# Performance work log

Hardware: AMD Instinct MI355X
Metric: run time of the kernel (lower is better)

The kernel has to match this reference:

```python
import jax, jax.numpy as jnp
import numpy as np

LOG_2PI = float(np.log(2.0 * np.pi))


def setup_inputs() -> dict:
    key = jax.random.key(0)
    k1, k2, k3 = jax.random.split(key, 3)
    N, M, D = 8192, 4096, 784
    samples = jax.random.normal(k1, (N, D), dtype=jnp.float32)
    x = jax.random.normal(k2, (M, D), dtype=jnp.float32)
    # per-feature std, kept away from zero for numerical sanity
    std = jax.random.uniform(k3, (D,), dtype=jnp.float32, minval=0.5, maxval=1.5)
    return {"samples": samples, "x": x, "std": std}


def reference(samples, x, std):
    # Diagonal-Gaussian mixture log-prob:
    #   logp[n, m] = sum_d [ -0.5*((s_nd - x_md)/std_d)^2 - 0.5*log(2*pi) - log(std_d) ]
    # computed via the ||u||^2 + ||v||^2 - 2 u.v identity on std-scaled vectors
    # (mathematically identical to the torch broadcast, without the (N,M,D) tensor).
    N, D = samples.shape
    M = x.shape[0]
    u = samples / std  # (N, D)
    v = x / std        # (M, D)
    sq_dist = (
        jnp.sum(u * u, axis=1)[:, None]
        + jnp.sum(v * v, axis=1)[None, :]
        - 2.0 * jnp.einsum("nd,md->nm", u, v)
    )  # (N, M)
    log_const = -0.5 * D * LOG_2PI - jnp.sum(jnp.log(std))
    log_prob = -0.5 * sq_dist + log_const  # (N, M)
    # logsumexp over mixture components, minus log(M)
    return jax.nn.logsumexp(log_prob, axis=1) - jnp.log(jnp.asarray(M, dtype=samples.dtype))
```

## Files before the change

### kernel.cpp

```cpp
#include <hip/hip_runtime.h>
#include <cstdint>
#include <cstddef>


#define N_ROWS 8192
#define M_ROWS 4096
#define D_DIM  784
#define KPB    896
#define LOG2PI 1.8378770664093453f
#define LOGM   8.317766166719343f

typedef unsigned char u8;
typedef __attribute__((ext_vector_type(8))) int   i32x8;
typedef __attribute__((ext_vector_type(4))) float f32x4;

__device__ __forceinline__ void gld16(const u8* g, u8* l) {
    __builtin_amdgcn_global_load_lds(
        (__attribute__((address_space(1))) void*)(void*)g,
        (__attribute__((address_space(3))) void*)l, 16, 0, 0);
}

__global__ __launch_bounds__(256) void k_prep(const float* __restrict__ samples,
                                              const float* __restrict__ x,
                                              const float* __restrict__ stdv,
                                              u8* __restrict__ dst,
                                              float* __restrict__ norm) {
    const int wid = threadIdx.x >> 6, lane = threadIdx.x & 63;
    const int row0 = blockIdx.x * 32 + wid * 8;

    float4 rstd[4];
#pragma unroll
    for (int i = 0; i < 4; ++i) {
        int c = lane + 64 * i;
        rstd[i] = make_float4(1.f, 1.f, 1.f, 1.f);
        if (c < 196) {
            float4 d = ((const float4*)stdv)[c];
            rstd[i] = make_float4(1.f / d.x, 1.f / d.y, 1.f / d.z, 1.f / d.w);
        }
    }

    for (int rr = 0; rr < 8; ++rr) {
        const int row = row0 + rr;
        const float* src = (row < N_ROWS) ? samples + (size_t)row * D_DIM
                                          : x + (size_t)(row - N_ROWS) * D_DIM;
        unsigned* drow = (unsigned*)(dst + (size_t)row * KPB);
        float sq = 0.f;
#pragma unroll
        for (int i = 0; i < 4; ++i) {
            const int c = lane + 64 * i;
            if (c < 224) {
                unsigned p = 0;
                if (c < 196) {
                    float4 s = ((const float4*)src)[c];
                    float ux = s.x * rstd[i].x, uy = s.y * rstd[i].y;
                    float uz = s.z * rstd[i].z, uw = s.w * rstd[i].w;
                    p = __builtin_amdgcn_cvt_pk_fp8_f32(ux, uy, 0, false);
                    p = __builtin_amdgcn_cvt_pk_fp8_f32(uz, uw, p, true);
                    float r0 = __builtin_amdgcn_cvt_f32_fp8(p, 0);
                    float r1 = __builtin_amdgcn_cvt_f32_fp8(p, 1);
                    float r2 = __builtin_amdgcn_cvt_f32_fp8(p, 2);
                    float r3 = __builtin_amdgcn_cvt_f32_fp8(p, 3);
                    sq += r0 * r0 + r1 * r1 + r2 * r2 + r3 * r3;
                }
                drow[c] = p;
            }
        }
        for (int m = 32; m; m >>= 1) sq += __shfl_xor(sq, m);
        if (lane == 0) norm[row] = sq;
    }
}

__global__ __launch_bounds__(256) void k_gemm(const u8* __restrict__ U,
                                              const u8* __restrict__ V,
                                              const float* __restrict__ vnorm,
                                              float* __restrict__ pmax,
                                              float* __restrict__ psum) {
    __shared__ __align__(16) char smem[128 * 33 * 8];
    char* uT = smem;
    char* vT = smem + 16384;
    float2* part = (float2*)smem;

    const int tid = threadIdx.x;
    const int lane = tid & 63;
    const int wid = tid >> 6;
    const int waveRow = wid >> 1;
    const int waveCol = wid & 1;
    const int bCol = blockIdx.x;
    const int bRow = blockIdx.y;
    const int g = lane >> 4, rl = lane & 15;

    const int c0 = wid * 4;
    const int r = lane >> 3;
    const int gc = (lane & 7) ^ r;
    const u8* gu[4]; const u8* gv[4];
    u8* lu[4]; u8* lv[4];
#pragma unroll
    for (int t = 0; t < 4; ++t) {
        const int c = c0 + t;
        gu[t] = U + (size_t)(bRow * 128 + c * 8 + r) * KPB + gc * 16;
        gv[t] = V + (size_t)(bCol * 128 + c * 8 + r) * KPB + gc * 16;
        lu[t] = (u8*)(uT + c * 1024);
        lv[t] = (u8*)(vT + c * 1024);
    }

    const int key = rl & 7;
    const int sA0 = ((2 * g)     ^ key) * 16;
    const int sA1 = ((2 * g + 1) ^ key) * 16;
    const char* aBase = uT + (waveRow * 64 + rl) * 128;
    const char* bBase = vT + (waveCol * 64 + rl) * 128;

    f32x4 acc[4][4];
#pragma unroll
    for (int i = 0; i < 4; ++i)
#pragma unroll
        for (int j = 0; j < 4; ++j) acc[i][j] = (f32x4){0.f, 0.f, 0.f, 0.f};

    for (int kt = 0; kt < KPB / 128; ++kt) {
        const int k0 = kt * 128;
#pragma unroll
        for (int t = 0; t < 4; ++t) gld16(gu[t] + k0, lu[t]);
#pragma unroll
        for (int t = 0; t < 4; ++t) gld16(gv[t] + k0, lv[t]);
        __syncthreads();

        i32x8 a[4], b[4];
#pragma unroll
        for (int i = 0; i < 4; ++i) {
            const char* p = aBase + i * 16 * 128;
            int4 lo = *(const int4*)(p + sA0);
            int4 hi = *(const int4*)(p + sA1);
            a[i] = (i32x8){lo.x, lo.y, lo.z, lo.w, hi.x, hi.y, hi.z, hi.w};
        }
#pragma unroll
        for (int j = 0; j < 4; ++j) {
            const char* p = bBase + j * 16 * 128;
            int4 lo = *(const int4*)(p + sA0);
            int4 hi = *(const int4*)(p + sA1);
            b[j] = (i32x8){lo.x, lo.y, lo.z, lo.w, hi.x, hi.y, hi.z, hi.w};
        }
#pragma unroll
        for (int i = 0; i < 4; ++i)
#pragma unroll
            for (int j = 0; j < 4; ++j)
                acc[i][j] = __builtin_amdgcn_mfma_scale_f32_16x16x128_f8f6f4(
                    a[i], b[j], acc[i][j], 0 , 0 ,
                    0, 127 , 0, 127 );

        __syncthreads();
    }

    float vn[4];
#pragma unroll
    for (int j = 0; j < 4; ++j) vn[j] = vnorm[bCol * 128 + waveCol * 64 + j * 16 + rl];

    const int prow0 = waveRow * 64 + g * 4;
    const int pcol = waveCol * 16 + rl;
#pragma unroll
    for (int i = 0; i < 4; ++i) {
#pragma unroll
        for (int rg = 0; rg < 4; ++rg) {
            float w0 = acc[i][0][rg] - 0.5f * vn[0];
            float w1 = acc[i][1][rg] - 0.5f * vn[1];
            float w2 = acc[i][2][rg] - 0.5f * vn[2];
            float w3 = acc[i][3][rg] - 0.5f * vn[3];
            float m = fmaxf(fmaxf(w0, w1), fmaxf(w2, w3));
            float s = __expf(w0 - m) + __expf(w1 - m) + __expf(w2 - m) + __expf(w3 - m);
            part[(prow0 + i * 16 + rg) * 33 + pcol] = make_float2(m, s);
        }
    }
    __syncthreads();
    if (tid < 128) {
        const float2* p = part + tid * 33;
        float m = p[0].x;
#pragma unroll
        for (int c = 1; c < 32; ++c) m = fmaxf(m, p[c].x);
        float s = 0.f;
#pragma unroll
        for (int c = 0; c < 32; ++c) { float2 q = p[c]; s += q.y * __expf(q.x - m); }
        size_t grow = (size_t)(bRow * 128 + tid);
        pmax[grow * 32 + bCol] = m;
        psum[grow * 32 + bCol] = s;
    }
}

__global__ __launch_bounds__(256) void k_final(const float* __restrict__ pmax,
                                               const float* __restrict__ psum,
                                               const float* __restrict__ norm,
                                               const float* __restrict__ stdv,
                                               float* __restrict__ out) {
    __shared__ float wsum[4];
    const int t = threadIdx.x;
    float ls = 0.f;
    for (int d = t; d < D_DIM; d += 256) ls += logf(stdv[d]);
    for (int m = 32; m; m >>= 1) ls += __shfl_xor(ls, m);
    if ((t & 63) == 0) wsum[t >> 6] = ls;
    __syncthreads();
    const float logc = -0.5f * (float)D_DIM * LOG2PI - (wsum[0] + wsum[1] + wsum[2] + wsum[3]);

    const int n = blockIdx.x * 256 + t;
    const float* pm = pmax + (size_t)n * 32;
    const float* ps = psum + (size_t)n * 32;
    float gm = pm[0];
#pragma unroll
    for (int c = 1; c < 32; ++c) gm = fmaxf(gm, pm[c]);
    float S = 0.f;
#pragma unroll
    for (int c = 0; c < 32; ++c) S += ps[c] * __expf(pm[c] - gm);
    out[n] = gm + logf(S) - 0.5f * norm[n] + logc - LOGM;
}

extern "C" void kernel_launch(void* const* d_in, const int* in_sizes, int n_in,
                              void* d_out, int out_size, void* d_ws, size_t ws_size,
                              hipStream_t stream) {
    const float* samples = (const float*)d_in[0];
    const float* x       = (const float*)d_in[1];
    const float* stdv    = (const float*)d_in[2];
    float* out = (float*)d_out;

    char* ws = (char*)d_ws;
    u8*    U    = (u8*)ws;
    u8*    V    = (u8*)(ws + 7340032);
    float* norm = (float*)(ws + 11010048);
    float* pmax = (float*)(ws + 11059200);
    float* psum = (float*)(ws + 12107776);

    k_prep<<<(N_ROWS + M_ROWS) / 32, 256, 0, stream>>>(samples, x, stdv, U, norm);
    k_gemm<<<dim3(M_ROWS / 128, N_ROWS / 128), 256, 0, stream>>>(U, V, norm + N_ROWS, pmax, psum);
    k_final<<<N_ROWS / 256, 256, 0, stream>>>(pmax, psum, norm, stdv, out);
}
```

Baseline: 135.8 us.

## Double-buffer fp8 GEMM LDS tiles with async prefetch and new swizzle layout

The GEMM kernel now prefetches the next 128-wide K tile into a second LDS buffer while MFMAs run on the current one. It waits with explicit vmcnt counts and raw barriers instead of full syncthreads, and lays LDS out as two 64-byte halves with a new XOR swizzle. The prep kernel processes 2 rows per wave instead of 8, launching four times as many blocks to raise parallelism. LDS use grows to 64 KB per block, which may limit occupancy, and the hand-coded waitcnt values must match the number of outstanding loads.

Result: faster. 124.3 us (-8.5%).

```diff
diff --git a/kernel.cpp b/kernel.cpp
--- a/kernel.cpp
+++ b/kernel.cpp
@@ -26,7 +26,7 @@
                                               u8* __restrict__ dst,
                                               float* __restrict__ norm) {
     const int wid = threadIdx.x >> 6, lane = threadIdx.x & 63;
-    const int row0 = blockIdx.x * 32 + wid * 8;
+    const int row0 = blockIdx.x * 8 + wid * 2;
 
     float4 rstd[4];
 #pragma unroll
@@ -39,7 +39,8 @@
         }
     }
 
-    for (int rr = 0; rr < 8; ++rr) {
+#pragma unroll
+    for (int rr = 0; rr < 2; ++rr) {
         const int row = row0 + rr;
         const float* src = (row < N_ROWS) ? samples + (size_t)row * D_DIM
                                           : x + (size_t)(row - N_ROWS) * D_DIM;
@@ -75,9 +76,7 @@
                                               const float* __restrict__ vnorm,
                                               float* __restrict__ pmax,
                                               float* __restrict__ psum) {
-    __shared__ __align__(16) char smem[128 * 33 * 8];
-    char* uT = smem;
-    char* vT = smem + 16384;
+    __shared__ __align__(16) char smem[65536];
     float2* part = (float2*)smem;
 
     const int tid = threadIdx.x;
@@ -89,25 +88,22 @@
     const int bRow = blockIdx.y;
     const int g = lane >> 4, rl = lane & 15;
 
-    const int c0 = wid * 4;
-    const int r = lane >> 3;
-    const int gc = (lane & 7) ^ r;
-    const u8* gu[4]; const u8* gv[4];
-    u8* lu[4]; u8* lv[4];
+    const int r16 = lane >> 2, sl = lane & 3;
+    const int gc16 = sl ^ ((r16 >> 1) & 3);
+    const u8* ga[4]; const u8* gb[4]; int loff[4];
 #pragma unroll
     for (int t = 0; t < 4; ++t) {
-        const int c = c0 + t;
-        gu[t] = U + (size_t)(bRow * 128 + c * 8 + r) * KPB + gc * 16;
-        gv[t] = V + (size_t)(bCol * 128 + c * 8 + r) * KPB + gc * 16;
-        lu[t] = (u8*)(uT + c * 1024);
-        lv[t] = (u8*)(vT + c * 1024);
-    }
-
-    const int key = rl & 7;
-    const int sA0 = ((2 * g)     ^ key) * 16;
-    const int sA1 = ((2 * g + 1) ^ key) * 16;
-    const char* aBase = uT + (waveRow * 64 + rl) * 128;
-    const char* bBase = vT + (waveCol * 64 + rl) * 128;
+        const int lin = wid * 4 + t, h = lin & 1, rg = lin >> 1;
+        ga[t] = U + (size_t)(bRow * 128 + rg * 16 + r16) * KPB + h * 64 + gc16 * 16;
+        gb[t] = V + (size_t)(bCol * 128 + rg * 16 + r16) * KPB + h * 64 + gc16 * 16;
+        loff[t] = h * 8192 + rg * 1024;
+    }
+
+    const int key = (rl >> 1) & 3;
+    const int hA = (g >> 1) * 8192;
+    const int slotLo = (2 * (g & 1)) ^ key;
+    const int aoff = hA + (waveRow * 64 + rl) * 64 + slotLo * 16;
+    const int boff = 16384 + hA + (waveCol * 64 + rl) * 64 + slotLo * 16;
 
     f32x4 acc[4][4];
 #pragma unroll
@@ -115,28 +111,39 @@
 #pragma unroll
         for (int j = 0; j < 4; ++j) acc[i][j] = (f32x4){0.f, 0.f, 0.f, 0.f};
 
-    for (int kt = 0; kt < KPB / 128; ++kt) {
-        const int k0 = kt * 128;
-#pragma unroll
-        for (int t = 0; t < 4; ++t) gld16(gu[t] + k0, lu[t]);
-#pragma unroll
-        for (int t = 0; t < 4; ++t) gld16(gv[t] + k0, lv[t]);
-        __syncthreads();
-
+#pragma unroll
+    for (int t = 0; t < 4; ++t) gld16(ga[t], (u8*)(smem + loff[t]));
+#pragma unroll
+    for (int t = 0; t < 4; ++t) gld16(gb[t], (u8*)(smem + 16384 + loff[t]));
+
+#pragma unroll
+    for (int kt = 0; kt < 7; ++kt) {
+        if (kt < 6) {
+            char* nb = smem + ((kt + 1) & 1) * 32768;
+            const int k1 = (kt + 1) * 128;
+#pragma unroll
+            for (int t = 0; t < 4; ++t) gld16(ga[t] + k1, (u8*)(nb + loff[t]));
+#pragma unroll
+            for (int t = 0; t < 4; ++t) gld16(gb[t] + k1, (u8*)(nb + 16384 + loff[t]));
+            __builtin_amdgcn_s_waitcnt(0x0F78);
+        } else {
+            __builtin_amdgcn_s_waitcnt(0x0F70);
+        }
+        __builtin_amdgcn_s_barrier();
+
+        const char* base = smem + (kt & 1) * 32768;
         i32x8 a[4], b[4];
 #pragma unroll
         for (int i = 0; i < 4; ++i) {
-            const char* p = aBase + i * 16 * 128;
-            int4 lo = *(const int4*)(p + sA0);
-            int4 hi = *(const int4*)(p + sA1);
-            a[i] = (i32x8){lo.x, lo.y, lo.z, lo.w, hi.x, hi.y, hi.z, hi.w};
+            int4 L = *(const int4*)(base + (aoff + i * 1024));
+            int4 H = *(const int4*)(base + ((aoff + i * 1024) ^ 16));
+            a[i] = (i32x8){L.x, L.y, L.z, L.w, H.x, H.y, H.z, H.w};
         }
 #pragma unroll
         for (int j = 0; j < 4; ++j) {
-            const char* p = bBase + j * 16 * 128;
-            int4 lo = *(const int4*)(p + sA0);
-            int4 hi = *(const int4*)(p + sA1);
-            b[j] = (i32x8){lo.x, lo.y, lo.z, lo.w, hi.x, hi.y, hi.z, hi.w};
+            int4 L = *(const int4*)(base + (boff + j * 1024));
+            int4 H = *(const int4*)(base + ((boff + j * 1024) ^ 16));
+            b[j] = (i32x8){L.x, L.y, L.z, L.w, H.x, H.y, H.z, H.w};
         }
 #pragma unroll
         for (int i = 0; i < 4; ++i)
@@ -146,8 +153,9 @@
                     a[i], b[j], acc[i][j], 0 , 0 ,
                     0, 127 , 0, 127 );
 
-        __syncthreads();
-    }
+        __builtin_amdgcn_s_barrier();
+    }
+    __syncthreads();
 
     float vn[4];
 #pragma unroll
@@ -224,7 +232,7 @@
     float* pmax = (float*)(ws + 11059200);
     float* psum = (float*)(ws + 12107776);
 
-    k_prep<<<(N_ROWS + M_ROWS) / 32, 256, 0, stream>>>(samples, x, stdv, U, norm);
+    k_prep<<<(N_ROWS + M_ROWS) / 8, 256, 0, stream>>>(samples, x, stdv, U, norm);
     k_gemm<<<dim3(M_ROWS / 128, N_ROWS / 128), 256, 0, stream>>>(U, V, norm + N_ROWS, pmax, psum);
     k_final<<<N_ROWS / 256, 256, 0, stream>>>(pmax, psum, norm, stdv, out);
 }
```
